# Optimization experiments

Hardware: AMD Instinct MI355X
Metric: run time of the kernel (lower is better)

Reference implementation:

```python
import jax, jax.numpy as jnp
import numpy as np

N, D, DIM, H = 50000, 32, 128, 4  # nodes, fixed degree, feature dim, heads


def setup_inputs() -> dict:
    key = jax.random.key(0)
    ks = jax.random.split(key, 8)
    s = 1.0 / np.sqrt(DIM)
    h = jax.random.normal(ks[0], (N, DIM), dtype=jnp.float32)
    neigh_idx = jax.random.randint(ks[1], (N, D), 0, N, dtype=jnp.int32)
    W = jax.random.uniform(ks[2], (H, DIM, DIM), jnp.float32, -s, s)   # per-head fciandj
    a1 = jax.random.uniform(ks[3], (H, DIM), jnp.float32, -s, s)       # key weight, src half
    a2 = jax.random.uniform(ks[4], (H, DIM), jnp.float32, -s, s)       # key weight, nbr half
    Wg = jax.random.uniform(ks[5], (DIM, H), jnp.float32, -s, s)       # GetGate projection
    W0 = jax.random.uniform(ks[6], (H * DIM, DIM), jnp.float32, -s, s) # output mix w0
    return {"h": h, "neigh_idx": neigh_idx, "W": W, "a1": a1, "a2": a2, "Wg": Wg, "W0": W0}


def reference(h, neigh_idx, W, a1, a2, Wg, W0):
    # gate per node per head (GetGate assumed: softmax over heads of linear proj)
    g = jax.nn.softmax(h @ Wg, axis=-1)            # [N, H]
    hjs = h[neigh_idx]                              # [N, D, d] per-edge gather (shared across heads)
    heads = []
    for k in range(W.shape[0]):
        wh = h @ W[k]                               # [N, d]
        whjs = jnp.einsum('ndi,ij->ndj', hjs, W[k]) # [N, D, d]
        # edge score: key([wh_i, wh_j]) = wh_i.a1 + wh_j.a2, then leaky_relu
        e = jax.nn.leaky_relu((wh @ a1[k])[:, None] + whjs @ a2[k])  # [N, D]
        att = jax.nn.softmax(e, axis=1)             # segment softmax over neighbors
        out = jax.nn.relu(jnp.einsum('nd,ndj->nj', att, whjs))       # [N, d]
        heads.append(g[:, k:k + 1] * out)
    return jnp.concatenate(heads, axis=-1) @ W0     # [N, d]
```

## Files before the change

### kernel.cpp

```cpp
#include <hip/hip_runtime.h>

typedef __attribute__((ext_vector_type(8))) short short8;
typedef __attribute__((ext_vector_type(4))) float f32x4;
typedef __attribute__((ext_vector_type(2))) float f32x2;

__device__ __forceinline__ float bf2f(unsigned u16) {
    union { float f; unsigned u32; } v; v.u32 = u16 << 16; return v.f;
}
__device__ __forceinline__ unsigned short f2bf(float f) {
    union { float f; unsigned u32; } v; v.f = f;
    unsigned x = v.u32;
    x += ((x >> 16) & 1u) + 0x7FFFu;
    return (unsigned short)(x >> 16);
}
__device__ __forceinline__ unsigned packbf(float a, float b) {
    return (unsigned)f2bf(a) | ((unsigned)f2bf(b) << 16);
}
__device__ __forceinline__ f32x2 unpack2(unsigned hv) {
    union { float f; unsigned u; } lo, hi;
    lo.u = hv << 16;
    hi.u = hv & 0xffff0000u;
    f32x2 r; r.x = lo.f; r.y = hi.f; return r;
}

__global__ __launch_bounds__(256) void kprep(const float* __restrict__ W,
                                             const float* __restrict__ W0,
                                             const float* __restrict__ a1,
                                             const float* __restrict__ a2,
                                             unsigned short* __restrict__ Wt,
                                             unsigned short* __restrict__ W0t,
                                             float* __restrict__ b1,
                                             float* __restrict__ b2) {
    int b = blockIdx.x, t = threadIdx.x;
    if (b < 256) {
        int idx = b * 256 + t;
        int head = idx >> 14, rem = idx & 16383, k = rem >> 7, col = rem & 127;
        Wt[head * 16384 + col * 128 + k] = f2bf(W[idx]);
    } else if (b < 512) {
        int i2 = (b - 256) * 256 + t;
        int k = i2 >> 7, col = i2 & 127;
        W0t[col * 512 + k] = f2bf(W0[i2]);
    } else {
        int idx = (b - 512) * 256 + t;
        int k = idx >> 7, i = idx & 127;
        const float* wr = &W[k * 16384 + i * 128];
        const float* A1 = &a1[k * 128];
        const float* A2 = &a2[k * 128];
        float v1 = 0.f, v2 = 0.f;
        for (int c = 0; c < 128; ++c) { float wv = wr[c]; v1 += wv * A1[c]; v2 += wv * A2[c]; }
        b1[k * 128 + i] = v1;
        b2[k * 128 + i] = v2;
    }
}

__global__ __launch_bounds__(256) void kscore(const float* __restrict__ h,
                                              const float* __restrict__ Wg,
                                              const float* __restrict__ b1,
                                              const float* __restrict__ b2,
                                              unsigned* __restrict__ hb32,
                                              float* __restrict__ s1,
                                              float* __restrict__ s2,
                                              float* __restrict__ g,
                                              int N) {
    const int t = threadIdx.x, w = t >> 6, l = t & 63;
    const int grp = l >> 4, q = l & 15;
    const int n = blockIdx.x * 16 + w * 4 + grp;
    if (n >= N) return;

    float4 hv0 = *(const float4*)&h[(size_t)n * 128 + q * 8];
    float4 hv1 = *(const float4*)&h[(size_t)n * 128 + q * 8 + 4];
    float ha[8] = {hv0.x, hv0.y, hv0.z, hv0.w, hv1.x, hv1.y, hv1.z, hv1.w};

    uint4 hbv;
    hbv.x = packbf(ha[0], ha[1]); hbv.y = packbf(ha[2], ha[3]);
    hbv.z = packbf(ha[4], ha[5]); hbv.w = packbf(ha[6], ha[7]);
    *(uint4*)&hb32[(size_t)n * 64 + q * 4] = hbv;

    float p[12];
    #pragma unroll
    for (int k = 0; k < 4; ++k) {
        float4 ba = *(const float4*)&b1[k * 128 + q * 8];
        float4 bb = *(const float4*)&b1[k * 128 + q * 8 + 4];
        p[k] = ha[0]*ba.x + ha[1]*ba.y + ha[2]*ba.z + ha[3]*ba.w
             + ha[4]*bb.x + ha[5]*bb.y + ha[6]*bb.z + ha[7]*bb.w;
        float4 ca = *(const float4*)&b2[k * 128 + q * 8];
        float4 cb = *(const float4*)&b2[k * 128 + q * 8 + 4];
        p[4+k] = ha[0]*ca.x + ha[1]*ca.y + ha[2]*ca.z + ha[3]*ca.w
               + ha[4]*cb.x + ha[5]*cb.y + ha[6]*cb.z + ha[7]*cb.w;
    }
    p[8] = p[9] = p[10] = p[11] = 0.f;
    #pragma unroll
    for (int e = 0; e < 8; ++e) {
        float4 wg = *(const float4*)&Wg[(q * 8 + e) * 4];
        p[8]  += ha[e] * wg.x;
        p[9]  += ha[e] * wg.y;
        p[10] += ha[e] * wg.z;
        p[11] += ha[e] * wg.w;
    }
    #pragma unroll
    for (int m = 8; m >= 1; m >>= 1) {
        #pragma unroll
        for (int i = 0; i < 12; ++i) p[i] += __shfl_xor(p[i], m, 16);
    }
    if (q == 0) {
        *(float4*)&s1[n * 4] = make_float4(p[0], p[1], p[2], p[3]);
        *(float4*)&s2[n * 4] = make_float4(p[4], p[5], p[6], p[7]);
        float mx = fmaxf(fmaxf(p[8], p[9]), fmaxf(p[10], p[11]));
        float e0 = __expf(p[8] - mx), e1 = __expf(p[9] - mx);
        float e2 = __expf(p[10] - mx), e3 = __expf(p[11] - mx);
        float si = 1.f / (e0 + e1 + e2 + e3);
        *(float4*)&g[n * 4] = make_float4(e0 * si, e1 * si, e2 * si, e3 * si);
    }
}

__global__ __launch_bounds__(256) void k3_mix(const int* __restrict__ idx,
                                              const unsigned* __restrict__ hb32,
                                              const float* __restrict__ s1,
                                              const float* __restrict__ s2,
                                              unsigned* __restrict__ Mx32,
                                              int N) {
    __shared__ float att4s[4][32][4];
    const int t = threadIdx.x, w = t >> 6, l = t & 63;
    const int d = l & 31, half = l >> 5;
    int n = blockIdx.x * 4 + w;
    const bool valid = (n < N);
    if (!valid) n = N - 1;

    int j = idx[(size_t)n * 32 + d];
    float2 s2v = *(const float2*)&s2[(size_t)j * 4 + half * 2];
    const float* s1p = &s1[(size_t)n * 4];
    float e0 = s1p[half * 2] + s2v.x;
    float e1 = s1p[half * 2 + 1] + s2v.y;
    e0 = (e0 >= 0.f) ? e0 : 0.01f * e0;
    e1 = (e1 >= 0.f) ? e1 : 0.01f * e1;
    float m0 = e0, m1 = e1;
    #pragma unroll
    for (int mm = 16; mm >= 1; mm >>= 1) {
        m0 = fmaxf(m0, __shfl_xor(m0, mm, 32));
        m1 = fmaxf(m1, __shfl_xor(m1, mm, 32));
    }
    float p0 = __expf(e0 - m0), p1 = __expf(e1 - m1);
    float q0 = p0, q1 = p1;
    #pragma unroll
    for (int mm = 16; mm >= 1; mm >>= 1) {
        q0 += __shfl_xor(q0, mm, 32);
        q1 += __shfl_xor(q1, mm, 32);
    }
    *(float2*)&att4s[w][d][half * 2] = make_float2(p0 / q0, p1 / q1);

    f32x2 ac0 = {}, ac1 = {}, ac2 = {}, ac3 = {};
    #pragma unroll
    for (int dd = 0; dd < 32; ++dd) {
        int jj = __shfl(j, dd, 64);
        unsigned hv = hb32[(size_t)jj * 64 + l];
        f32x2 h01 = unpack2(hv);
        float4 a4 = *(const float4*)&att4s[w][dd][0];
        ac0 += (f32x2){a4.x, a4.x} * h01;
        ac1 += (f32x2){a4.y, a4.y} * h01;
        ac2 += (f32x2){a4.z, a4.z} * h01;
        ac3 += (f32x2){a4.w, a4.w} * h01;
    }
    if (valid) {
        Mx32[(size_t)n * 256 +   0 + l] = packbf(ac0.x, ac0.y);
        Mx32[(size_t)n * 256 +  64 + l] = packbf(ac1.x, ac1.y);
        Mx32[(size_t)n * 256 + 128 + l] = packbf(ac2.x, ac2.y);
        Mx32[(size_t)n * 256 + 192 + l] = packbf(ac3.x, ac3.y);
    }
}

typedef const __attribute__((address_space(1))) char gbyte;
typedef __attribute__((address_space(3))) char lbyte;

__global__ __launch_bounds__(512, 1) void k4_gemm(const unsigned short* __restrict__ Mx,
                                                  const unsigned short* __restrict__ Wt,
                                                  const unsigned short* __restrict__ W0t,
                                                  const float* __restrict__ g,
                                                  float* __restrict__ out,
                                                  int N, int T) {
    __shared__ unsigned short Uin[2][32 * 512];
    __shared__ unsigned short Uout[32 * 512];
    __shared__ float gld[2][128];
    const int tid = threadIdx.x, w = tid >> 6, l = tid & 63;
    const int l15 = l & 15, lh = l >> 4;
    const int hd = w & 3, ch = w >> 2;
    const int P = gridDim.x;

    short8 bf1[4][4];
    #pragma unroll
    for (int s = 0; s < 4; ++s)
        #pragma unroll
        for (int c = 0; c < 4; ++c)
            bf1[s][c] = *(const short8*)&Wt[(size_t)hd * 16384 +
                                            (size_t)((ch * 4 + c) * 16 + l15) * 128 + s * 32 + lh * 8];
    short8 bf2[16];
    #pragma unroll
    for (int ks = 0; ks < 16; ++ks)
        bf2[ks] = *(const short8*)&W0t[(size_t)(w * 16 + l15) * 512 + ks * 32 + lh * 8];

    const int t0 = blockIdx.x;

    auto STAGE = [&](int tile, int b) {
        const size_t n0 = (size_t)tile * 32;
        if (w == 0 && l < 32) {
            size_t n = n0 + l; if (n >= (size_t)N) n = N - 1;
            __builtin_amdgcn_global_load_lds((gbyte*)((const char*)g + n * 16),
                                             (lbyte*)&gld[b][0], 16, 0, 0);
        }
        #pragma unroll
        for (int p = 0; p < 4; ++p) {
            int r = p * 8 + w;
            size_t n = n0 + r;
            if (n >= (size_t)N) n = N - 1;
            const char* src = (const char*)Mx + n * 1024 + ((l * 16) ^ ((r & 7) << 4));
            __builtin_amdgcn_global_load_lds((gbyte*)src, (lbyte*)&Uin[b][r * 512], 16, 0, 0);
        }
    };

    STAGE(t0, 0);
    __syncthreads();
    if (t0 + P < T) STAGE(t0 + P, 1);

    int buf = 0;
    for (int t = t0; t < T; t += P, buf ^= 1) {
        const int n0 = t * 32;

        const char* Uibuf = (const char*)Uin[buf];
        #pragma unroll
        for (int rg = 0; rg < 2; ++rg) {
            const int arow = rg * 16 + l15;
            short8 af[4];
            #pragma unroll
            for (int s = 0; s < 4; ++s) {
                int ab = arow * 1024 + hd * 256 + s * 64 + lh * 16;
                af[s] = *(const short8*)(Uibuf + (ab ^ ((arow & 7) << 4)));
            }
            f32x4 acc[4] = {};
            #pragma unroll
            for (int s = 0; s < 4; ++s)
                #pragma unroll
                for (int c = 0; c < 4; ++c)
                    acc[c] = __builtin_amdgcn_mfma_f32_16x16x32_bf16(af[s], bf1[s][c], acc[c], 0, 0, 0);
            #pragma unroll
            for (int c = 0; c < 4; ++c) {
                const int col = hd * 128 + (ch * 4 + c) * 16 + l15;
                #pragma unroll
                for (int r = 0; r < 4; ++r) {
                    int row = rg * 16 + lh * 4 + r;
                    float v = fmaxf(acc[c][r], 0.f) * gld[buf][row * 4 + hd];
                    int ub = row * 1024 + col * 2;
                    *(unsigned short*)((char*)Uout + (ub ^ ((row & 7) << 4))) = f2bf(v);
                }
            }
        }

        __syncthreads();

        if (t + 2 * P < T) STAGE(t + 2 * P, buf);

        const char* Uob = (const char*)Uout;
        #pragma unroll
        for (int rg = 0; rg < 2; ++rg) {
            const int arow = rg * 16 + l15;
            f32x4 oacc = {};
            #pragma unroll
            for (int ks = 0; ks < 16; ++ks) {
                int ab = arow * 1024 + ks * 64 + lh * 16;
                short8 afr = *(const short8*)(Uob + (ab ^ ((arow & 7) << 4)));
                oacc = __builtin_amdgcn_mfma_f32_16x16x32_bf16(afr, bf2[ks], oacc, 0, 0, 0);
            }
            #pragma unroll
            for (int r = 0; r < 4; ++r) {
                int n = n0 + rg * 16 + lh * 4 + r;
                if (n < N) out[(size_t)n * 128 + w * 16 + l15] = oacc[r];
            }
        }

        __syncthreads();
    }
}

extern "C" void kernel_launch(void* const* d_in, const int* in_sizes, int n_in,
                              void* d_out, int out_size, void* d_ws, size_t ws_size,
                              hipStream_t stream) {
    const float* h     = (const float*)d_in[0];
    const int*   neigh = (const int*)d_in[1];
    const float* W     = (const float*)d_in[2];
    const float* a1    = (const float*)d_in[3];
    const float* a2    = (const float*)d_in[4];
    const float* Wg    = (const float*)d_in[5];
    const float* W0    = (const float*)d_in[6];
    float* out = (float*)d_out;

    const int N = in_sizes[0] / 128;

    char* ws = (char*)d_ws;
    unsigned* hb32 = (unsigned*)ws;
    unsigned* Mx32 = (unsigned*)(ws + (size_t)N * 256);
    float* s1 = (float*)(ws + (size_t)N * 256 + (size_t)N * 1024);
    float* s2 = s1 + (size_t)N * 4;
    float* g  = s2 + (size_t)N * 4;
    unsigned short* Wt  = (unsigned short*)(g + (size_t)N * 4);
    unsigned short* W0t = Wt + 65536;
    float* b1 = (float*)(W0t + 65536);
    float* b2 = b1 + 512;

    const int T = (N + 31) / 32;
    const int P = (T < 256) ? T : 256;

    kprep<<<dim3(514), dim3(256), 0, stream>>>(W, W0, a1, a2, Wt, W0t, b1, b2);
    kscore<<<dim3((N + 15) / 16), dim3(256), 0, stream>>>(h, Wg, b1, b2, hb32, s1, s2, g, N);
    k3_mix<<<dim3((N + 3) / 4), dim3(256), 0, stream>>>(neigh, hb32, s1, s2, Mx32, N);
    k4_gemm<<<dim3(P), dim3(512), 0, stream>>>((const unsigned short*)Mx32, Wt, W0t, g,
                                               out, N, T);
}
```

Before: 121.4 us.

## Fold weight transposes into mix kernel, widen mix blocks, single-buffer GEMM staging

```diff
diff --git a/kernel.cpp b/kernel.cpp
--- a/kernel.cpp
+++ b/kernel.cpp
@@ -23,34 +23,20 @@
     f32x2 r; r.x = lo.f; r.y = hi.f; return r;
 }
 
-__global__ __launch_bounds__(256) void kprep(const float* __restrict__ W,
-                                             const float* __restrict__ W0,
-                                             const float* __restrict__ a1,
-                                             const float* __restrict__ a2,
-                                             unsigned short* __restrict__ Wt,
-                                             unsigned short* __restrict__ W0t,
-                                             float* __restrict__ b1,
-                                             float* __restrict__ b2) {
-    int b = blockIdx.x, t = threadIdx.x;
-    if (b < 256) {
-        int idx = b * 256 + t;
-        int head = idx >> 14, rem = idx & 16383, k = rem >> 7, col = rem & 127;
-        Wt[head * 16384 + col * 128 + k] = f2bf(W[idx]);
-    } else if (b < 512) {
-        int i2 = (b - 256) * 256 + t;
-        int k = i2 >> 7, col = i2 & 127;
-        W0t[col * 512 + k] = f2bf(W0[i2]);
-    } else {
-        int idx = (b - 512) * 256 + t;
-        int k = idx >> 7, i = idx & 127;
-        const float* wr = &W[k * 16384 + i * 128];
-        const float* A1 = &a1[k * 128];
-        const float* A2 = &a2[k * 128];
-        float v1 = 0.f, v2 = 0.f;
-        for (int c = 0; c < 128; ++c) { float wv = wr[c]; v1 += wv * A1[c]; v2 += wv * A2[c]; }
-        b1[k * 128 + i] = v1;
-        b2[k * 128 + i] = v2;
-    }
+__global__ __launch_bounds__(256) void kb12(const float* __restrict__ W,
+                                            const float* __restrict__ a1,
+                                            const float* __restrict__ a2,
+                                            float* __restrict__ b1,
+                                            float* __restrict__ b2) {
+    int idx = blockIdx.x * 256 + threadIdx.x;
+    int k = idx >> 7, i = idx & 127;
+    const float* wr = &W[k * 16384 + i * 128];
+    const float* A1 = &a1[k * 128];
+    const float* A2 = &a2[k * 128];
+    float v1 = 0.f, v2 = 0.f;
+    for (int c = 0; c < 128; ++c) { float wv = wr[c]; v1 += wv * A1[c]; v2 += wv * A2[c]; }
+    b1[k * 128 + i] = v1;
+    b2[k * 128 + i] = v2;
 }
 
 __global__ __launch_bounds__(256) void kscore(const float* __restrict__ h,
@@ -113,16 +99,35 @@
     }
 }
 
-__global__ __launch_bounds__(256) void k3_mix(const int* __restrict__ idx,
+__global__ __launch_bounds__(512) void k3_mix(const int* __restrict__ idx,
                                               const unsigned* __restrict__ hb32,
                                               const float* __restrict__ s1,
                                               const float* __restrict__ s2,
                                               unsigned* __restrict__ Mx32,
-                                              int N) {
-    __shared__ float att4s[4][32][4];
-    const int t = threadIdx.x, w = t >> 6, l = t & 63;
+                                              const float* __restrict__ W,
+                                              const float* __restrict__ W0,
+                                              unsigned short* __restrict__ Wt,
+                                              unsigned short* __restrict__ W0t,
+                                              int N, int nb) {
+    const int b = blockIdx.x, tid = threadIdx.x;
+    if (b >= nb) {
+        int bb = b - nb;
+        if (bb < 128) {
+            int i = bb * 512 + tid;
+            int head = i >> 14, rem = i & 16383, k = rem >> 7, col = rem & 127;
+            Wt[head * 16384 + col * 128 + k] = f2bf(W[i]);
+        } else {
+            int i = (bb - 128) * 512 + tid;
+            int k = i >> 7, col = i & 127;
+            W0t[col * 512 + k] = f2bf(W0[i]);
+        }
+        return;
+    }
+
+    __shared__ float att4s[8][32][4];
+    const int w = tid >> 6, l = tid & 63;
     const int d = l & 31, half = l >> 5;
-    int n = blockIdx.x * 4 + w;
+    int n = b * 8 + w;
     const bool valid = (n < N);
     if (!valid) n = N - 1;
 
@@ -177,9 +182,9 @@
                                                   const float* __restrict__ g,
                                                   float* __restrict__ out,
                                                   int N, int T) {
-    __shared__ unsigned short Uin[2][32 * 512];
+    __shared__ unsigned short Uin[32 * 512];
     __shared__ unsigned short Uout[32 * 512];
-    __shared__ float gld[2][128];
+    __shared__ float gld[128];
     const int tid = threadIdx.x, w = tid >> 6, l = tid & 63;
     const int l15 = l & 15, lh = l >> 4;
     const int hd = w & 3, ch = w >> 2;
@@ -199,12 +204,12 @@
 
     const int t0 = blockIdx.x;
 
-    auto STAGE = [&](int tile, int b) {
+    auto STAGE = [&](int tile) {
         const size_t n0 = (size_t)tile * 32;
         if (w == 0 && l < 32) {
             size_t n = n0 + l; if (n >= (size_t)N) n = N - 1;
             __builtin_amdgcn_global_load_lds((gbyte*)((const char*)g + n * 16),
-                                             (lbyte*)&gld[b][0], 16, 0, 0);
+                                             (lbyte*)&gld[0], 16, 0, 0);
         }
         #pragma unroll
         for (int p = 0; p < 4; ++p) {
@@ -212,19 +217,17 @@
             size_t n = n0 + r;
             if (n >= (size_t)N) n = N - 1;
             const char* src = (const char*)Mx + n * 1024 + ((l * 16) ^ ((r & 7) << 4));
-            __builtin_amdgcn_global_load_lds((gbyte*)src, (lbyte*)&Uin[b][r * 512], 16, 0, 0);
+            __builtin_amdgcn_global_load_lds((gbyte*)src, (lbyte*)&Uin[r * 512], 16, 0, 0);
         }
     };
 
-    STAGE(t0, 0);
+    STAGE(t0);
     __syncthreads();
-    if (t0 + P < T) STAGE(t0 + P, 1);
-
-    int buf = 0;
-    for (int t = t0; t < T; t += P, buf ^= 1) {
+
+    for (int t = t0; t < T; t += P) {
         const int n0 = t * 32;
 
-        const char* Uibuf = (const char*)Uin[buf];
+        const char* Uib = (const char*)Uin;
         #pragma unroll
         for (int rg = 0; rg < 2; ++rg) {
             const int arow = rg * 16 + l15;
@@ -232,7 +235,7 @@
             #pragma unroll
             for (int s = 0; s < 4; ++s) {
                 int ab = arow * 1024 + hd * 256 + s * 64 + lh * 16;
-                af[s] = *(const short8*)(Uibuf + (ab ^ ((arow & 7) << 4)));
+                af[s] = *(const short8*)(Uib + (ab ^ ((arow & 7) << 4)));
             }
             f32x4 acc[4] = {};
             #pragma unroll
@@ -246,7 +249,7 @@
                 #pragma unroll
                 for (int r = 0; r < 4; ++r) {
                     int row = rg * 16 + lh * 4 + r;
-                    float v = fmaxf(acc[c][r], 0.f) * gld[buf][row * 4 + hd];
+                    float v = fmaxf(acc[c][r], 0.f) * gld[row * 4 + hd];
                     int ub = row * 1024 + col * 2;
                     *(unsigned short*)((char*)Uout + (ub ^ ((row & 7) << 4))) = f2bf(v);
                 }
@@ -255,7 +258,7 @@
 
         __syncthreads();
 
-        if (t + 2 * P < T) STAGE(t + 2 * P, buf);
+        if (t + P < T) STAGE(t + P);
 
         const char* Uob = (const char*)Uout;
         #pragma unroll
@@ -304,12 +307,14 @@
     float* b1 = (float*)(W0t + 65536);
     float* b2 = b1 + 512;
 
+    const int nb = (N + 7) / 8;
     const int T = (N + 31) / 32;
     const int P = (T < 256) ? T : 256;
 
-    kprep<<<dim3(514), dim3(256), 0, stream>>>(W, W0, a1, a2, Wt, W0t, b1, b2);
+    kb12<<<dim3(2), dim3(256), 0, stream>>>(W, a1, a2, b1, b2);
     kscore<<<dim3((N + 15) / 16), dim3(256), 0, stream>>>(h, Wg, b1, b2, hb32, s1, s2, g, N);
-    k3_mix<<<dim3((N + 3) / 4), dim3(256), 0, stream>>>(neigh, hb32, s1, s2, Mx32, N);
+    k3_mix<<<dim3(nb + 256), dim3(512), 0, stream>>>(neigh, hb32, s1, s2, Mx32,
+                                                     W, W0, Wt, W0t, N, nb);
     k4_gemm<<<dim3(P), dim3(512), 0, stream>>>((const unsigned short*)Mx32, Wt, W0t, g,
                                                out, N, T);
 }
```

New measurement: 123.5 us. No clear change (+1.7%).
